# Kernel tuning notes

Measured on AMD Instinct MI355X. Metric: run time of the kernel, lower is better.

Reference implementation:

```python
import jax, jax.numpy as jnp
import numpy as np

IS, OS, H = 168, 24, 256           # input window, output horizon, state_hsize
TAU, MAXIMUM = 0.1, 1.0            # tau parameter (non-grad) and series maximum
DILS = [[1, 4], [16, 64]]          # ResidualDRNN groups of dilations


def _lstm(x, wih, whh, bih, bhh):
    """Single-layer LSTM over time-major x: (T, B, C). PyTorch gate order i,f,g,o."""
    def step(carry, xt):
        h, c = carry
        g = xt @ wih.T + h @ whh.T + (bih + bhh)
        i, f, gg, o = jnp.split(g, 4, axis=-1)
        c = jax.nn.sigmoid(f) * c + jax.nn.sigmoid(i) * jnp.tanh(gg)
        h = jax.nn.sigmoid(o) * jnp.tanh(c)
        return (h, c), h
    h0 = jnp.zeros((x.shape[1], H), x.dtype)
    _, hs = jax.lax.scan(step, (h0, h0), x)
    return hs


def _dilated_lstm(x, d, p):
    """Standard DRNN layer: pad T to multiple of d, interleave time into batch, run LSTM."""
    T, B, C = x.shape
    n = -(-T // d)
    xp = jnp.pad(x, ((0, n * d - T), (0, 0), (0, 0)))
    hd = _lstm(xp.reshape(n, d * B, C), *p)
    return hd.reshape(n * d, B, H)[:T]


def _forward(train, init_lev_sm, lstm_params, nl_w, nl_b, sc_w, sc_b):
    B, T = train.shape
    a = jax.nn.sigmoid(init_lev_sm[0])            # lev_sms (idxs are all 0 -> same scalar)
    floor = TAU * MAXIMUM                          # tau * maximum
    # --- exponential-smoothing level recurrence (sequential) ---
    lev0 = jnp.maximum(train[:, 0], floor)
    def step(lev, xt):
        new = jnp.maximum(a * xt + (1.0 - a) * lev, floor)
        return new, new
    _, rest = jax.lax.scan(step, lev0, train[:, 1:].T)
    levs = jnp.concatenate([lev0[None], rest], axis=0).T   # [B, T]
    # --- windowed normalization ---
    w_idx = jnp.arange(IS - 1, T)                           # W = T - IS + 1 window ends
    in_win = train[:, (w_idx - IS + 1)[:, None] + jnp.arange(IS)[None, :]]
    in_win = (in_win / levs[:, w_idx][:, :, None]).transpose(1, 0, 2)    # [W, B, IS]
    o_idx = jnp.arange(IS - 1, T - OS)                      # W_out = T - OS - IS + 1
    out_win = train[:, (o_idx + 1)[:, None] + jnp.arange(OS)[None, :]]
    out_win = (out_win / levs[:, o_idx][:, :, None]).transpose(1, 0, 2)  # [W_out, B, OS]
    # --- ResidualDRNN stack on window_input[:-OS] (time-major: windows are the sequence) ---
    x = in_win[:-OS]
    li = 0
    for g, dils in enumerate(DILS):
        residual = x
        h = x
        for d in dils:
            h = _dilated_lstm(h, d, lstm_params[li])
            li += 1
        x = h + residual if g > 0 else h                    # dropout p=0 -> identity
    x = jnp.tanh(x @ nl_w.T + nl_b)                         # add_nl_layer
    pred = x @ sc_w.T + sc_b                                # scoring
    return pred, out_win


def setup_inputs() -> dict:
    key = jax.random.key(0)
    ks = list(jax.random.split(key, 32))
    B, T = 32, 1024
    inp = {
        "train": jax.random.uniform(ks[0], (B, T), jnp.float32, 0.05, 1.0),
        "val": jax.random.uniform(ks[1], (B, T), jnp.float32, 0.05, 1.0),
        "test": jax.random.uniform(ks[2], (B, T), jnp.float32, 0.05, 1.0),
        "idxs": jnp.zeros((B,), jnp.int32),
        "init_lev_sm": jnp.array([0.5], jnp.float32),
    }
    sizes = [IS, H, H, H]  # input feature size of each of the 4 DRNN layers
    k = 3
    s = 1.0 / np.sqrt(H)
    for i, cin in enumerate(sizes):
        inp[f"wih{i}"] = jax.random.uniform(ks[k], (4 * H, cin), jnp.float32, -s, s); k += 1
        inp[f"whh{i}"] = jax.random.uniform(ks[k], (4 * H, H), jnp.float32, -s, s); k += 1
        inp[f"bih{i}"] = jax.random.uniform(ks[k], (4 * H,), jnp.float32, -s, s); k += 1
        inp[f"bhh{i}"] = jax.random.uniform(ks[k], (4 * H,), jnp.float32, -s, s); k += 1
    inp["nl_w"] = jax.random.uniform(ks[k], (H, H), jnp.float32, -s, s); k += 1
    inp["nl_b"] = jnp.zeros((H,), jnp.float32)
    inp["sc_w"] = jax.random.uniform(ks[k], (OS, H), jnp.float32, -s, s); k += 1
    inp["sc_b"] = jnp.zeros((OS,), jnp.float32)
    return inp


def reference(train, val, test, idxs, init_lev_sm,
              wih0, whh0, bih0, bhh0, wih1, whh1, bih1, bhh1,
              wih2, whh2, bih2, bhh2, wih3, whh3, bih3, bhh3,
              nl_w, nl_b, sc_w, sc_b):
    lstm_params = [(wih0, whh0, bih0, bhh0), (wih1, whh1, bih1, bhh1),
                   (wih2, whh2, bih2, bhh2), (wih3, whh3, bih3, bhh3)]
    # training path (validating=False, testing=False): only `train` is used
    return _forward(train, init_lev_sm, lstm_params, nl_w, nl_b, sc_w, sc_b)
```

## Files before the change

### kernel.cpp

```cpp
#include <hip/hip_runtime.h>
#include <hip/hip_fp16.h>
#include <math.h>

#define TT 833
#define GDIM 1024

typedef _Float16 f16x8 __attribute__((ext_vector_type(8)));
typedef float    f32x4 __attribute__((ext_vector_type(4)));

__device__ __forceinline__ float sigm(float x){ return 1.f/(1.f+expf(-x)); }

#if __has_builtin(__builtin_amdgcn_sdot4)
__device__ __forceinline__ int sdot4(unsigned a, unsigned b, int c){
  return __builtin_amdgcn_sdot4((int)a, (int)b, c, false);
}
#else
__device__ __forceinline__ int sdot4(unsigned a, unsigned b, int c){
  int ai = (int)a, bi = (int)b;
  c += ((ai<<24)>>24)*((bi<<24)>>24);
  c += ((ai<<16)>>24)*((bi<<16)>>24);
  c += ((ai<<8)>>24)*((bi<<8)>>24);
  c += (ai>>24)*(bi>>24);
  return c;
}
#endif

__global__ void levels_k(const float* __restrict__ train, const float* __restrict__ ism,
                         float* __restrict__ levs){
  int b = threadIdx.x;
  if (b >= 32) return;
  float a = 1.f/(1.f+expf(-ism[0]));
  const float* tr = train + b*1024;
  float* lv = levs + b*1024;
  float lev = fmaxf(tr[0], 0.1f);
  lv[0] = lev;
  for (int t = 1; t < 1024; ++t){
    lev = fmaxf(a*tr[t] + (1.f-a)*lev, 0.1f);
    lv[t] = lev;
  }
}

__global__ void win_x_k(const float* __restrict__ train, const float* __restrict__ levs,
                        float* __restrict__ x0){
  int idx = blockIdx.x*256 + threadIdx.x;
  int i = idx % 168;
  int r = idx / 168;
  int b = r & 31;
  int t = r >> 5;
  x0[idx] = train[b*1024 + t + i] / levs[b*1024 + t + 167];
}

__global__ void win_out_k(const float* __restrict__ train, const float* __restrict__ levs,
                          float* __restrict__ ow){
  int idx = blockIdx.x*256 + threadIdx.x;
  int o = idx % 24;
  int r = idx / 24;
  int b = r & 31;
  int t = r >> 5;
  ow[idx] = train[b*1024 + 168 + t + o] / levs[b*1024 + t + 167];
}

__global__ void packq_k(const float* __restrict__ w, uint4* __restrict__ wq,
                        float* __restrict__ sc){
  int g = blockIdx.x*256 + threadIdx.x;
  if (g >= 1024) return;
  const float* row = w + (size_t)g*256;
  float amax = 0.f;
  for (int k = 0; k < 256; ++k) amax = fmaxf(amax, fabsf(row[k]));
  amax = fmaxf(amax, 1e-20f);
  float s = amax/127.f, inv = 127.f/amax;
  sc[g] = s;
  for (int k16 = 0; k16 < 16; ++k16){
    union { uint4 u; signed char b[16]; } r;
    #pragma unroll
    for (int j = 0; j < 16; ++j){
      float q = rintf(row[k16*16 + j]*inv);
      q = fminf(fmaxf(q, -127.f), 127.f);
      r.b[j] = (signed char)q;
    }
    wq[(size_t)k16*1024 + g] = r.u;
  }
}

__global__ __launch_bounds__(256) void proj_mfma(
    const float* __restrict__ A, const float* __restrict__ W,
    const float* __restrict__ b1, const float* __restrict__ b2,
    float* __restrict__ C, int Mout, int K, int N, int dil, int act)
{
  __shared__ _Float16 As[128*40];
  __shared__ _Float16 Bs[128*40];
  const int tid = threadIdx.x;
  const int lane = tid & 63;
  const int w = tid >> 6, wr = w >> 1, wc = w & 1;
  const int m0 = blockIdx.y << 7, n0 = blockIdx.x << 7;

  const int rowA = tid >> 1;
  int srcrow;
  {
    int m = m0 + rowA;
    if (dil == 0) srcrow = (m < Mout) ? m : -1;
    else {
      int rows = dil << 5;
      int j = m / rows;
      int q = m - j*rows;
      int t = j*dil + (q >> 5);
      srcrow = (t < TT) ? ((t << 5) + (q & 31)) : -1;
    }
  }
  const int halfsel = tid & 1;
  const int nrow = n0 + rowA;

  f32x4 acc[4][4];
  #pragma unroll
  for (int i = 0; i < 4; ++i)
    #pragma unroll
    for (int j = 0; j < 4; ++j) acc[i][j] = (f32x4){0.f,0.f,0.f,0.f};

  const int nkt = (K + 31) >> 5;
  for (int kt = 0; kt < nkt; ++kt){
    const int k0 = (kt << 5) + halfsel*16;
    {
      union { uint4 u[2]; _Float16 h[16]; } tmp;
      if (srcrow >= 0 && k0 + 16 <= K){
        const float* s = A + (size_t)srcrow*K + k0;
        #pragma unroll
        for (int j = 0; j < 4; ++j){
          float4 v = *reinterpret_cast<const float4*>(s + j*4);
          tmp.h[j*4+0]=(_Float16)v.x; tmp.h[j*4+1]=(_Float16)v.y;
          tmp.h[j*4+2]=(_Float16)v.z; tmp.h[j*4+3]=(_Float16)v.w;
        }
      } else {
        const float* s = (srcrow >= 0) ? A + (size_t)srcrow*K : nullptr;
        #pragma unroll
        for (int j = 0; j < 16; ++j){
          int kk = k0 + j;
          tmp.h[j] = (s && kk < K) ? (_Float16)s[kk] : (_Float16)0.f;
        }
      }
      uint4* dst = reinterpret_cast<uint4*>(&As[rowA*40 + halfsel*16]);
      dst[0] = tmp.u[0]; dst[1] = tmp.u[1];
    }
    {
      union { uint4 u[2]; _Float16 h[16]; } tmp;
      if (k0 + 16 <= K){
        const float* s = W + (size_t)nrow*K + k0;
        #pragma unroll
        for (int j = 0; j < 4; ++j){
          float4 v = *reinterpret_cast<const float4*>(s + j*4);
          tmp.h[j*4+0]=(_Float16)v.x; tmp.h[j*4+1]=(_Float16)v.y;
          tmp.h[j*4+2]=(_Float16)v.z; tmp.h[j*4+3]=(_Float16)v.w;
        }
      } else {
        const float* s = W + (size_t)nrow*K;
        #pragma unroll
        for (int j = 0; j < 16; ++j){
          int kk = k0 + j;
          tmp.h[j] = (kk < K) ? (_Float16)s[kk] : (_Float16)0.f;
        }
      }
      uint4* dst = reinterpret_cast<uint4*>(&Bs[rowA*40 + halfsel*16]);
      dst[0] = tmp.u[0]; dst[1] = tmp.u[1];
    }
    __syncthreads();
    {
      const int kg = lane >> 4, r16 = lane & 15;
      f16x8 af[4], bf[4];
      #pragma unroll
      for (int mi = 0; mi < 4; ++mi)
        af[mi] = *reinterpret_cast<const f16x8*>(&As[(wr*64 + mi*16 + r16)*40 + kg*8]);
      #pragma unroll
      for (int nj = 0; nj < 4; ++nj)
        bf[nj] = *reinterpret_cast<const f16x8*>(&Bs[(wc*64 + nj*16 + r16)*40 + kg*8]);
      #pragma unroll
      for (int mi = 0; mi < 4; ++mi)
        #pragma unroll
        for (int nj = 0; nj < 4; ++nj)
          acc[mi][nj] = __builtin_amdgcn_mfma_f32_16x16x32_f16(af[mi], bf[nj], acc[mi][nj], 0, 0, 0);
    }
    __syncthreads();
  }
  #pragma unroll
  for (int mi = 0; mi < 4; ++mi){
    #pragma unroll
    for (int p = 0; p < 4; ++p){
      int mrow = m0 + wr*64 + mi*16 + (lane >> 4)*4 + p;
      if (mrow >= Mout) continue;
      #pragma unroll
      for (int nj = 0; nj < 4; ++nj){
        int ncol = n0 + wc*64 + nj*16 + (lane & 15);
        float v = acc[mi][nj][p] + b1[ncol] + (b2 ? b2[ncol] : 0.f);
        if (act) v = tanhf(v);
        C[(size_t)mrow*N + ncol] = v;
      }
    }
  }
}

template<int NR>
__global__ __launch_bounds__(1024) void srecr_k(
    const uint4* __restrict__ wq, const float* __restrict__ scale,
    const float* __restrict__ Gin,
    float* __restrict__ out, const float* __restrict__ res,
    int nsteps, int d, int rowsTotal)
{
  __shared__ unsigned int hq[NR][64];
  __shared__ float psum[NR][1024];
  __shared__ float cst[NR][256];
  const int tid = threadIdx.x;
  const int q0 = blockIdx.x*NR;
  const float sg = scale[tid]*(1.f/127.f);
  uint4 wr_[16];
  #pragma unroll
  for (int k = 0; k < 16; ++k) wr_[k] = wq[(size_t)k*1024 + tid];
  for (int e = tid; e < NR*64; e += 1024) (&hq[0][0])[e] = 0u;
  for (int e = tid; e < NR*256; e += 1024) (&cst[0][0])[e] = 0.f;
  __syncthreads();

  for (int step = 0; step < nsteps; ++step){
    float gin[NR];
    const float* gbase = Gin + ((size_t)step*rowsTotal + q0)*GDIM;
    #pragma unroll
    for (int rr = 0; rr < NR; ++rr) gin[rr] = gbase[rr*GDIM + tid];
    int acc[NR];
    #pragma unroll
    for (int rr = 0; rr < NR; ++rr) acc[rr] = 0;

    #pragma unroll
    for (int k16 = 0; k16 < 16; ++k16){
      uint4 w = wr_[k16];
      #pragma unroll
      for (int rr = 0; rr < NR; ++rr){
        uint4 h4 = *reinterpret_cast<const uint4*>(&hq[rr][4*k16]);
        acc[rr] = sdot4(w.x, h4.x, acc[rr]);
        acc[rr] = sdot4(w.y, h4.y, acc[rr]);
        acc[rr] = sdot4(w.z, h4.z, acc[rr]);
        acc[rr] = sdot4(w.w, h4.w, acc[rr]);
      }
    }
    #pragma unroll
    for (int rr = 0; rr < NR; ++rr) psum[rr][tid] = fmaf((float)acc[rr], sg, gin[rr]);
    __syncthreads();
    for (int e = tid; e < NR*256; e += 1024){
      int rr = e >> 8, j = e & 255;
      float iv = psum[rr][j];
      float fv = psum[rr][j + 256];
      float gv = psum[rr][j + 512];
      float ov = psum[rr][j + 768];
      float c = cst[rr][j];
      c = sigm(fv)*c + sigm(iv)*tanhf(gv);
      float h = sigm(ov)*tanhf(c);
      cst[rr][j] = c;
      int qh = (int)rintf(h*127.f);
      reinterpret_cast<signed char*>(&hq[rr][0])[j] = (signed char)qh;
      int q = q0 + rr;
      int tg = step*d + (q >> 5);
      if (tg < TT){
        size_t oi = ((size_t)tg*32 + (q & 31))*256 + j;
        out[oi] = res ? (h + res[oi]) : h;
      }
    }
    __syncthreads();
  }
}

template<int NR>
__global__ __launch_bounds__(1024) void srecq_k(
    const uint4* __restrict__ wq, const float* __restrict__ scale,
    const float* __restrict__ Gin,
    float* __restrict__ out, const float* __restrict__ res,
    int nsteps, int d, int rowsTotal)
{
  __shared__ unsigned int hq[NR][64];
  __shared__ float psum[NR][1024];
  __shared__ float cst[NR][256];
  const int tid = threadIdx.x;
  const int q0 = blockIdx.x*NR;
  const float sg = scale[tid]*(1.f/127.f);
  for (int e = tid; e < NR*64; e += 1024) (&hq[0][0])[e] = 0u;
  for (int e = tid; e < NR*256; e += 1024) (&cst[0][0])[e] = 0.f;
  __syncthreads();

  for (int step = 0; step < nsteps; ++step){
    float gin[NR];
    const float* gbase = Gin + ((size_t)step*rowsTotal + q0)*GDIM;
    #pragma unroll
    for (int rr = 0; rr < NR; ++rr) gin[rr] = gbase[rr*GDIM + tid];
    int acc[NR];
    #pragma unroll
    for (int rr = 0; rr < NR; ++rr) acc[rr] = 0;

    #pragma unroll 4
    for (int k16 = 0; k16 < 16; ++k16){
      uint4 w = wq[(size_t)k16*1024 + tid];
      #pragma unroll
      for (int rr = 0; rr < NR; ++rr){
        uint4 h4 = *reinterpret_cast<const uint4*>(&hq[rr][4*k16]);
        acc[rr] = sdot4(w.x, h4.x, acc[rr]);
        acc[rr] = sdot4(w.y, h4.y, acc[rr]);
        acc[rr] = sdot4(w.z, h4.z, acc[rr]);
        acc[rr] = sdot4(w.w, h4.w, acc[rr]);
      }
    }
    #pragma unroll
    for (int rr = 0; rr < NR; ++rr) psum[rr][tid] = fmaf((float)acc[rr], sg, gin[rr]);
    __syncthreads();
    for (int e = tid; e < NR*256; e += 1024){
      int rr = e >> 8, j = e & 255;
      float iv = psum[rr][j];
      float fv = psum[rr][j + 256];
      float gv = psum[rr][j + 512];
      float ov = psum[rr][j + 768];
      float c = cst[rr][j];
      c = sigm(fv)*c + sigm(iv)*tanhf(gv);
      float h = sigm(ov)*tanhf(c);
      cst[rr][j] = c;
      int qh = (int)rintf(h*127.f);
      reinterpret_cast<signed char*>(&hq[rr][0])[j] = (signed char)qh;
      int q = q0 + rr;
      int tg = step*d + (q >> 5);
      if (tg < TT){
        size_t oi = ((size_t)tg*32 + (q & 31))*256 + j;
        out[oi] = res ? (h + res[oi]) : h;
      }
    }
    __syncthreads();
  }
}

__global__ __launch_bounds__(256) void sc_head(const float* __restrict__ xt, const float* __restrict__ w,
                        const float* __restrict__ bias, float* __restrict__ outp, int M){
  __shared__ float arow[8][256];
  int m0 = blockIdx.x << 3;
  int tid = threadIdx.x;
  #pragma unroll
  for (int i = 0; i < 8; ++i){
    int e = tid + (i << 8);
    int r = e >> 8, k = e & 255;
    arow[r][k] = (m0 + r < M) ? xt[(size_t)(m0 + r)*256 + k] : 0.f;
  }
  __syncthreads();
  int r = tid >> 5, n = tid & 31;
  if (n < 24 && (m0 + r) < M){
    float acc = bias[n];
    const float* wr = w + n*256;
    #pragma unroll 8
    for (int k = 0; k < 256; ++k) acc = fmaf(arow[r][k], wr[k], acc);
    outp[(size_t)(m0 + r)*24 + n] = acc;
  }
}

extern "C" void kernel_launch(void* const* d_in, const int* in_sizes, int n_in,
                              void* d_out, int out_size, void* d_ws, size_t ws_size,
                              hipStream_t stream){
  const float* train = (const float*)d_in[0];
  const float* ism   = (const float*)d_in[4];
  const float* wih[4] = {(const float*)d_in[5], (const float*)d_in[9], (const float*)d_in[13], (const float*)d_in[17]};
  const float* whh[4] = {(const float*)d_in[6], (const float*)d_in[10], (const float*)d_in[14], (const float*)d_in[18]};
  const float* bih[4] = {(const float*)d_in[7], (const float*)d_in[11], (const float*)d_in[15], (const float*)d_in[19]};
  const float* bhh[4] = {(const float*)d_in[8], (const float*)d_in[12], (const float*)d_in[16], (const float*)d_in[20]};
  const float* nl_w = (const float*)d_in[21];
  const float* nl_b = (const float*)d_in[22];
  const float* sc_w = (const float*)d_in[23];
  const float* sc_b = (const float*)d_in[24];
  float* out = (float*)d_out;

  float* ws = (float*)d_ws;
  size_t off = 0;
  float* levs = ws + off;   off += 32768;
  uint4* wqk[4];
  for (int l = 0; l < 4; ++l){ wqk[l] = (uint4*)(ws + off); off += 65536; }
  float* sck[4];
  for (int l = 0; l < 4; ++l){ sck[l] = ws + off; off += 1024; }
  float* x0 = ws + off;     off += (size_t)26656*168;
  float* G  = ws + off;     off += (size_t)28672*1024;
  float* h0 = ws + off;     off += (size_t)26656*256;
  float* h1 = ws + off;     off += (size_t)26656*256;
  float* h2 = ws + off;     off += (size_t)26656*256;
  (void)ws_size; (void)in_sizes; (void)n_in; (void)out_size;

  levels_k<<<1, 64, 0, stream>>>(train, ism, levs);
  win_x_k<<<17493, 256, 0, stream>>>(train, levs, x0);
  win_out_k<<<2499, 256, 0, stream>>>(train, levs, out + 639744);
  for (int l = 0; l < 4; ++l)
    packq_k<<<4, 256, 0, stream>>>(whh[l], wqk[l], sck[l]);

  proj_mfma<<<dim3(8,209), 256, 0, stream>>>(x0, wih[0], bih[0], bhh[0], G, 26656, 168, 1024, 0, 0);
  srecr_k<1><<<32, 1024, 0, stream>>>(wqk[0], sck[0], G, h0, nullptr, 833, 1, 32);
  proj_mfma<<<dim3(8,209), 256, 0, stream>>>(h0, wih[1], bih[1], bhh[1], G, 26752, 256, 1024, 4, 0);
  srecr_k<1><<<128, 1024, 0, stream>>>(wqk[1], sck[1], G, h1, nullptr, 209, 4, 128);
  proj_mfma<<<dim3(8,212), 256, 0, stream>>>(h1, wih[2], bih[2], bhh[2], G, 27136, 256, 1024, 16, 0);
  srecr_k<2><<<256, 1024, 0, stream>>>(wqk[2], sck[2], G, h2, nullptr, 53, 16, 512);
  proj_mfma<<<dim3(8,224), 256, 0, stream>>>(h2, wih[3], bih[3], bhh[3], G, 28672, 256, 1024, 64, 0);
  srecq_k<8><<<256, 1024, 0, stream>>>(wqk[3], sck[3], G, h2, h1, 14, 64, 2048);
  proj_mfma<<<dim3(2,209), 256, 0, stream>>>(h2, nl_w, nl_b, nullptr, h0, 26656, 256, 256, 0, 1);
  sc_head<<<3332, 256, 0, stream>>>(h0, sc_w, sc_b, out, 26656);
}
```

Baseline: 1.992 ms.

## Interleave LSTM gates per unit, fuse cell update via shuffles, store gates in fp16

The gate rows of the input and recurrent weights are permuted so each group of 4 adjacent threads owns the i,f,g,o gates of one hidden unit. The cell update is then done in registers with wavefront shuffles instead of a shared-memory psum round trip, and a double-buffered h vector removes one barrier per step. The precomputed input projection G is stored in fp16 to halve its traffic, and the recurrence uses fast exp-based sigmoid and tanh. This adds weight-permutation kernels and lowers precision for the gate preactivations.

```diff
diff --git a/kernel.cpp b/kernel.cpp
--- a/kernel.cpp
+++ b/kernel.cpp
@@ -8,7 +8,7 @@
 typedef _Float16 f16x8 __attribute__((ext_vector_type(8)));
 typedef float    f32x4 __attribute__((ext_vector_type(4)));
 
-__device__ __forceinline__ float sigm(float x){ return 1.f/(1.f+expf(-x)); }
+__device__ __forceinline__ float sigm(float x){ return 1.f/(1.f+__expf(-x)); }
 
 #if __has_builtin(__builtin_amdgcn_sdot4)
 __device__ __forceinline__ int sdot4(unsigned a, unsigned b, int c){
@@ -24,6 +24,7 @@
   return c;
 }
 #endif
+
 
 __global__ void levels_k(const float* __restrict__ train, const float* __restrict__ ism,
                          float* __restrict__ levs){
@@ -60,16 +61,27 @@
   ow[idx] = train[b*1024 + 168 + t + o] / levs[b*1024 + t + 167];
 }
 
+__global__ void permw_k(const float* __restrict__ wih, const float* __restrict__ bih,
+                        const float* __restrict__ bhh, float* __restrict__ wP,
+                        float* __restrict__ bP, int K){
+  int t = blockIdx.x;
+  int g = ((t & 3) << 8) + (t >> 2);
+  for (int k = threadIdx.x; k < K; k += 256)
+    wP[(size_t)t*K + k] = wih[(size_t)g*K + k];
+  if (threadIdx.x == 0) bP[t] = bih[g] + bhh[g];
+}
+
 __global__ void packq_k(const float* __restrict__ w, uint4* __restrict__ wq,
                         float* __restrict__ sc){
-  int g = blockIdx.x*256 + threadIdx.x;
-  if (g >= 1024) return;
+  int t = blockIdx.x*256 + threadIdx.x;
+  if (t >= 1024) return;
+  int g = ((t & 3) << 8) + (t >> 2);
   const float* row = w + (size_t)g*256;
   float amax = 0.f;
   for (int k = 0; k < 256; ++k) amax = fmaxf(amax, fabsf(row[k]));
   amax = fmaxf(amax, 1e-20f);
   float s = amax/127.f, inv = 127.f/amax;
-  sc[g] = s;
+  sc[t] = s;
   for (int k16 = 0; k16 < 16; ++k16){
     union { uint4 u; signed char b[16]; } r;
     #pragma unroll
@@ -78,14 +90,14 @@
       q = fminf(fmaxf(q, -127.f), 127.f);
       r.b[j] = (signed char)q;
     }
-    wq[(size_t)k16*1024 + g] = r.u;
+    wq[(size_t)k16*1024 + t] = r.u;
   }
 }
 
 __global__ __launch_bounds__(256) void proj_mfma(
     const float* __restrict__ A, const float* __restrict__ W,
     const float* __restrict__ b1, const float* __restrict__ b2,
-    float* __restrict__ C, int Mout, int K, int N, int dil, int act)
+    float* __restrict__ C, int Mout, int K, int N, int dil, int act, int outHalf)
 {
   __shared__ _Float16 As[128*40];
   __shared__ _Float16 Bs[128*40];
@@ -190,7 +202,8 @@
         int ncol = n0 + wc*64 + nj*16 + (lane & 15);
         float v = acc[mi][nj][p] + b1[ncol] + (b2 ? b2[ncol] : 0.f);
         if (act) v = tanhf(v);
-        C[(size_t)mrow*N + ncol] = v;
+        if (outHalf) reinterpret_cast<__half*>(C)[(size_t)mrow*N + ncol] = __float2half(v);
+        else C[(size_t)mrow*N + ncol] = v;
       }
     }
   }
@@ -199,38 +212,110 @@
 template<int NR>
 __global__ __launch_bounds__(1024) void srecr_k(
     const uint4* __restrict__ wq, const float* __restrict__ scale,
-    const float* __restrict__ Gin,
+    const __half* __restrict__ Gin,
     float* __restrict__ out, const float* __restrict__ res,
     int nsteps, int d, int rowsTotal)
 {
-  __shared__ unsigned int hq[NR][64];
-  __shared__ float psum[NR][1024];
-  __shared__ float cst[NR][256];
+  __shared__ __align__(16) unsigned int hq[2][NR][64];
   const int tid = threadIdx.x;
+  const int lane = tid & 63;
+  const int base = lane & ~3;
+  const int kg = tid & 3;
+  const int j = tid >> 2;
   const int q0 = blockIdx.x*NR;
   const float sg = scale[tid]*(1.f/127.f);
   uint4 wr_[16];
   #pragma unroll
-  for (int k = 0; k < 16; ++k) wr_[k] = wq[(size_t)k*1024 + tid];
-  for (int e = tid; e < NR*64; e += 1024) (&hq[0][0])[e] = 0u;
-  for (int e = tid; e < NR*256; e += 1024) (&cst[0][0])[e] = 0.f;
+  for (int kk = 0; kk < 16; ++kk) wr_[kk] = wq[(size_t)kk*1024 + tid];
+  float c[NR];
+  #pragma unroll
+  for (int rr = 0; rr < NR; ++rr) c[rr] = 0.f;
+  for (int e = tid; e < 2*NR*64; e += 1024) (&hq[0][0][0])[e] = 0u;
   __syncthreads();
 
   for (int step = 0; step < nsteps; ++step){
+    const int cur = step & 1;
     float gin[NR];
-    const float* gbase = Gin + ((size_t)step*rowsTotal + q0)*GDIM;
-    #pragma unroll
-    for (int rr = 0; rr < NR; ++rr) gin[rr] = gbase[rr*GDIM + tid];
+    const __half* gbase = Gin + ((size_t)step*rowsTotal + q0)*GDIM;
+    #pragma unroll
+    for (int rr = 0; rr < NR; ++rr) gin[rr] = __half2float(gbase[rr*GDIM + tid]);
+    #pragma unroll
+    for (int rr = 0; rr < NR; ++rr){
+      int a0 = 0, a1 = 0;
+      #pragma unroll
+      for (int k16 = 0; k16 < 8; ++k16){
+        uint4 h4 = *reinterpret_cast<const uint4*>(&hq[cur][rr][4*k16]);
+        uint4 w = wr_[k16];
+        a0 = sdot4(w.x, h4.x, a0); a0 = sdot4(w.y, h4.y, a0);
+        a0 = sdot4(w.z, h4.z, a0); a0 = sdot4(w.w, h4.w, a0);
+        uint4 h4b = *reinterpret_cast<const uint4*>(&hq[cur][rr][4*(k16+8)]);
+        uint4 wb = wr_[k16+8];
+        a1 = sdot4(wb.x, h4b.x, a1); a1 = sdot4(wb.y, h4b.y, a1);
+        a1 = sdot4(wb.z, h4b.z, a1); a1 = sdot4(wb.w, h4b.w, a1);
+      }
+      float p = fmaf((float)(a0 + a1), sg, gin[rr]);
+      float px = (kg == 2) ? p + p : p;
+      float s = 1.f/(1.f + __expf(-px));
+      float a = (kg == 2) ? fmaf(2.f, s, -1.f) : s;
+      float iv = __shfl(a, base + 0);
+      float fv = __shfl(a, base + 1);
+      float gv = __shfl(a, base + 2);
+      float ov = __shfl(a, base + 3);
+      float cn = fmaf(fv, c[rr], iv*gv);
+      c[rr] = cn;
+      float e2 = __expf(-2.f*cn);
+      float h = ov*(1.f - e2)/(1.f + e2);
+      if (kg == 0){
+        int qh = (int)rintf(h*127.f);
+        reinterpret_cast<signed char*>(&hq[cur^1][rr][0])[j] = (signed char)qh;
+        int q = q0 + rr;
+        int tg = step*d + (q >> 5);
+        if (tg < TT){
+          size_t oi = ((size_t)tg*32 + (q & 31))*256 + j;
+          out[oi] = res ? (h + res[oi]) : h;
+        }
+      }
+    }
+    __syncthreads();
+  }
+}
+
+template<int NR>
+__global__ __launch_bounds__(1024) void srecq_k(
+    const uint4* __restrict__ wq, const float* __restrict__ scale,
+    const __half* __restrict__ Gin,
+    float* __restrict__ out, const float* __restrict__ res,
+    int nsteps, int d, int rowsTotal)
+{
+  __shared__ __align__(16) unsigned int hq[2][NR][64];
+  const int tid = threadIdx.x;
+  const int lane = tid & 63;
+  const int base = lane & ~3;
+  const int kg = tid & 3;
+  const int j = tid >> 2;
+  const int q0 = blockIdx.x*NR;
+  const float sg = scale[tid]*(1.f/127.f);
+  float c[NR];
+  #pragma unroll
+  for (int rr = 0; rr < NR; ++rr) c[rr] = 0.f;
+  for (int e = tid; e < 2*NR*64; e += 1024) (&hq[0][0][0])[e] = 0u;
+  __syncthreads();
+
+  for (int step = 0; step < nsteps; ++step){
+    const int cur = step & 1;
+    float gin[NR];
+    const __half* gbase = Gin + ((size_t)step*rowsTotal + q0)*GDIM;
+    #pragma unroll
+    for (int rr = 0; rr < NR; ++rr) gin[rr] = __half2float(gbase[rr*GDIM + tid]);
     int acc[NR];
     #pragma unroll
     for (int rr = 0; rr < NR; ++rr) acc[rr] = 0;
-
-    #pragma unroll
+    #pragma unroll 4
     for (int k16 = 0; k16 < 16; ++k16){
-      uint4 w = wr_[k16];
+      uint4 w = wq[(size_t)k16*1024 + tid];
       #pragma unroll
       for (int rr = 0; rr < NR; ++rr){
-        uint4 h4 = *reinterpret_cast<const uint4*>(&hq[rr][4*k16]);
+        uint4 h4 = *reinterpret_cast<const uint4*>(&hq[cur][rr][4*k16]);
         acc[rr] = sdot4(w.x, h4.x, acc[rr]);
         acc[rr] = sdot4(w.y, h4.y, acc[rr]);
         acc[rr] = sdot4(w.z, h4.z, acc[rr]);
@@ -238,89 +323,28 @@
       }
     }
     #pragma unroll
-    for (int rr = 0; rr < NR; ++rr) psum[rr][tid] = fmaf((float)acc[rr], sg, gin[rr]);
-    __syncthreads();
-    for (int e = tid; e < NR*256; e += 1024){
-      int rr = e >> 8, j = e & 255;
-      float iv = psum[rr][j];
-      float fv = psum[rr][j + 256];
-      float gv = psum[rr][j + 512];
-      float ov = psum[rr][j + 768];
-      float c = cst[rr][j];
-      c = sigm(fv)*c + sigm(iv)*tanhf(gv);
-      float h = sigm(ov)*tanhf(c);
-      cst[rr][j] = c;
-      int qh = (int)rintf(h*127.f);
-      reinterpret_cast<signed char*>(&hq[rr][0])[j] = (signed char)qh;
-      int q = q0 + rr;
-      int tg = step*d + (q >> 5);
-      if (tg < TT){
-        size_t oi = ((size_t)tg*32 + (q & 31))*256 + j;
-        out[oi] = res ? (h + res[oi]) : h;
-      }
-    }
-    __syncthreads();
-  }
-}
-
-template<int NR>
-__global__ __launch_bounds__(1024) void srecq_k(
-    const uint4* __restrict__ wq, const float* __restrict__ scale,
-    const float* __restrict__ Gin,
-    float* __restrict__ out, const float* __restrict__ res,
-    int nsteps, int d, int rowsTotal)
-{
-  __shared__ unsigned int hq[NR][64];
-  __shared__ float psum[NR][1024];
-  __shared__ float cst[NR][256];
-  const int tid = threadIdx.x;
-  const int q0 = blockIdx.x*NR;
-  const float sg = scale[tid]*(1.f/127.f);
-  for (int e = tid; e < NR*64; e += 1024) (&hq[0][0])[e] = 0u;
-  for (int e = tid; e < NR*256; e += 1024) (&cst[0][0])[e] = 0.f;
-  __syncthreads();
-
-  for (int step = 0; step < nsteps; ++step){
-    float gin[NR];
-    const float* gbase = Gin + ((size_t)step*rowsTotal + q0)*GDIM;
-    #pragma unroll
-    for (int rr = 0; rr < NR; ++rr) gin[rr] = gbase[rr*GDIM + tid];
-    int acc[NR];
-    #pragma unroll
-    for (int rr = 0; rr < NR; ++rr) acc[rr] = 0;
-
-    #pragma unroll 4
-    for (int k16 = 0; k16 < 16; ++k16){
-      uint4 w = wq[(size_t)k16*1024 + tid];
-      #pragma unroll
-      for (int rr = 0; rr < NR; ++rr){
-        uint4 h4 = *reinterpret_cast<const uint4*>(&hq[rr][4*k16]);
-        acc[rr] = sdot4(w.x, h4.x, acc[rr]);
-        acc[rr] = sdot4(w.y, h4.y, acc[rr]);
-        acc[rr] = sdot4(w.z, h4.z, acc[rr]);
-        acc[rr] = sdot4(w.w, h4.w, acc[rr]);
-      }
-    }
-    #pragma unroll
-    for (int rr = 0; rr < NR; ++rr) psum[rr][tid] = fmaf((float)acc[rr], sg, gin[rr]);
-    __syncthreads();
-    for (int e = tid; e < NR*256; e += 1024){
-      int rr = e >> 8, j = e & 255;
-      float iv = psum[rr][j];
-      float fv = psum[rr][j + 256];
-      float gv = psum[rr][j + 512];
-      float ov = psum[rr][j + 768];
-      float c = cst[rr][j];
-      c = sigm(fv)*c + sigm(iv)*tanhf(gv);
-      float h = sigm(ov)*tanhf(c);
-      cst[rr][j] = c;
-      int qh = (int)rintf(h*127.f);
-      reinterpret_cast<signed char*>(&hq[rr][0])[j] = (signed char)qh;
-      int q = q0 + rr;
-      int tg = step*d + (q >> 5);
-      if (tg < TT){
-        size_t oi = ((size_t)tg*32 + (q & 31))*256 + j;
-        out[oi] = res ? (h + res[oi]) : h;
+    for (int rr = 0; rr < NR; ++rr){
+      float p = fmaf((float)acc[rr], sg, gin[rr]);
+      float px = (kg == 2) ? p + p : p;
+      float s = 1.f/(1.f + __expf(-px));
+      float a = (kg == 2) ? fmaf(2.f, s, -1.f) : s;
+      float iv = __shfl(a, base + 0);
+      float fv = __shfl(a, base + 1);
+      float gv = __shfl(a, base + 2);
+      float ov = __shfl(a, base + 3);
+      float cn = fmaf(fv, c[rr], iv*gv);
+      c[rr] = cn;
+      float e2 = __expf(-2.f*cn);
+      float h = ov*(1.f - e2)/(1.f + e2);
+      if (kg == 0){
+        int qh = (int)rintf(h*127.f);
+        reinterpret_cast<signed char*>(&hq[cur^1][rr][0])[j] = (signed char)qh;
+        int q = q0 + rr;
+        int tg = step*d + (q >> 5);
+        if (tg < TT){
+          size_t oi = ((size_t)tg*32 + (q & 31))*256 + j;
+          out[oi] = res ? (h + res[oi]) : h;
+        }
       }
     }
     __syncthreads();
@@ -371,8 +395,12 @@
   for (int l = 0; l < 4; ++l){ wqk[l] = (uint4*)(ws + off); off += 65536; }
   float* sck[4];
   for (int l = 0; l < 4; ++l){ sck[l] = ws + off; off += 1024; }
+  float* wP[4];
+  for (int l = 0; l < 4; ++l){ wP[l] = ws + off; off += 262144; }
+  float* bP[4];
+  for (int l = 0; l < 4; ++l){ bP[l] = ws + off; off += 1024; }
   float* x0 = ws + off;     off += (size_t)26656*168;
-  float* G  = ws + off;     off += (size_t)28672*1024;
+  __half* G  = (__half*)(ws + off); off += (size_t)28672*1024/2;
   float* h0 = ws + off;     off += (size_t)26656*256;
   float* h1 = ws + off;     off += (size_t)26656*256;
   float* h2 = ws + off;     off += (size_t)26656*256;
@@ -381,17 +409,20 @@
   levels_k<<<1, 64, 0, stream>>>(train, ism, levs);
   win_x_k<<<17493, 256, 0, stream>>>(train, levs, x0);
   win_out_k<<<2499, 256, 0, stream>>>(train, levs, out + 639744);
-  for (int l = 0; l < 4; ++l)
+  const int Kin[4] = {168, 256, 256, 256};
+  for (int l = 0; l < 4; ++l){
     packq_k<<<4, 256, 0, stream>>>(whh[l], wqk[l], sck[l]);
-
-  proj_mfma<<<dim3(8,209), 256, 0, stream>>>(x0, wih[0], bih[0], bhh[0], G, 26656, 168, 1024, 0, 0);
+    permw_k<<<1024, 256, 0, stream>>>(wih[l], bih[l], bhh[l], wP[l], bP[l], Kin[l]);
+  }
+
+  proj_mfma<<<dim3(8,209), 256, 0, stream>>>(x0, wP[0], bP[0], nullptr, (float*)G, 26656, 168, 1024, 0, 0, 1);
   srecr_k<1><<<32, 1024, 0, stream>>>(wqk[0], sck[0], G, h0, nullptr, 833, 1, 32);
-  proj_mfma<<<dim3(8,209), 256, 0, stream>>>(h0, wih[1], bih[1], bhh[1], G, 26752, 256, 1024, 4, 0);
+  proj_mfma<<<dim3(8,209), 256, 0, stream>>>(h0, wP[1], bP[1], nullptr, (float*)G, 26752, 256, 1024, 4, 0, 1);
   srecr_k<1><<<128, 1024, 0, stream>>>(wqk[1], sck[1], G, h1, nullptr, 209, 4, 128);
-  proj_mfma<<<dim3(8,212), 256, 0, stream>>>(h1, wih[2], bih[2], bhh[2], G, 27136, 256, 1024, 16, 0);
+  proj_mfma<<<dim3(8,212), 256, 0, stream>>>(h1, wP[2], bP[2], nullptr, (float*)G, 27136, 256, 1024, 16, 0, 1);
   srecr_k<2><<<256, 1024, 0, stream>>>(wqk[2], sck[2], G, h2, nullptr, 53, 16, 512);
-  proj_mfma<<<dim3(8,224), 256, 0, stream>>>(h2, wih[3], bih[3], bhh[3], G, 28672, 256, 1024, 64, 0);
+  proj_mfma<<<dim3(8,224), 256, 0, stream>>>(h2, wP[3], bP[3], nullptr, (float*)G, 28672, 256, 1024, 64, 0, 1);
   srecq_k<8><<<256, 1024, 0, stream>>>(wqk[3], sck[3], G, h2, h1, 14, 64, 2048);
-  proj_mfma<<<dim3(2,209), 256, 0, stream>>>(h2, nl_w, nl_b, nullptr, h0, 26656, 256, 256, 0, 1);
+  proj_mfma<<<dim3(2,209), 256, 0, stream>>>(h2, nl_w, nl_b, nullptr, h0, 26656, 256, 256, 0, 1, 0);
   sc_head<<<3332, 256, 0, stream>>>(h0, sc_w, sc_b, out, 26656);
 }
```

After: 2.007 ms. Within noise of the previous version (+0.8%).
